# Performance work log

Hardware: AMD Instinct MI355X
Metric: run time of the kernel (lower is better)

## Reference

```python
import jax, jax.numpy as jnp
import numpy as np

D_MODEL, FF_DIM = 1024, 2048
N_SHARED, N_ROUTED, TOP_K = 1, 8, 2
BATCH, SEQ = 2, 2048


def setup_inputs() -> dict:
    key = jax.random.key(0)
    ks = jax.random.split(key, 8)
    init = lambda k, shape: (jax.random.normal(k, shape, jnp.float32) * 0.02)
    x = jax.random.normal(ks[0], (BATCH, SEQ, D_MODEL), jnp.float32)
    Wg = init(ks[1], (D_MODEL, N_ROUTED))                 # gate
    Ws1 = init(ks[2], (D_MODEL, FF_DIM))                  # shared expert (N_SHARED=1)
    Ws3 = init(ks[3], (D_MODEL, FF_DIM))
    Ws2 = init(ks[4], (FF_DIM, D_MODEL))
    We1 = init(ks[5], (N_ROUTED, D_MODEL, FF_DIM))        # routed experts, stacked
    We3 = init(ks[6], (N_ROUTED, D_MODEL, FF_DIM))
    We2 = init(ks[7], (N_ROUTED, FF_DIM, D_MODEL))
    return {"x": x, "Wg": Wg, "Ws1": Ws1, "Ws3": Ws3, "Ws2": Ws2,
            "We1": We1, "We3": We3, "We2": We2}


def reference(x, Wg, Ws1, Ws3, Ws2, We1, We3, We2):
    B, S, d = x.shape
    E = Wg.shape[1]
    xf = x.reshape(-1, d)                                  # [T, d]
    T = xf.shape[0]

    # sigmoid gate + top-k, normalized over selected experts
    gates = jax.nn.sigmoid(xf @ Wg)                        # [T, E]
    vals, idx = jax.lax.top_k(gates, TOP_K)                # [T, K]
    vals = vals / vals.sum(axis=-1, keepdims=True)
    # dense per-expert weights (scatter normalized top-k probs)
    w = jnp.zeros((T, E), x.dtype).at[jnp.arange(T)[:, None], idx].add(vals)  # [T, E]

    # shared expert SwiGLU
    shared = (jax.nn.silu(xf @ Ws1) * (xf @ Ws3)) @ Ws2    # [T, d]

    # routed experts: same math as the torch loop (compute all, mask by w)
    h = jax.nn.silu(jnp.einsum('td,edf->tef', xf, We1)) \
        * jnp.einsum('td,edf->tef', xf, We3)               # [T, E, ff]
    routed = jnp.einsum('tef,efd,te->td', h, We2, w)       # [T, d]

    out = (shared + routed) / (N_SHARED + TOP_K)
    return out.reshape(B, S, d)
```

## Files before the change

### kernel.cpp

```cpp
#include <hip/hip_runtime.h>
#include <stdint.h>

#define TTOK 4096
#define DM   1024
#define FF   2048
#define NE   8

typedef __attribute__((ext_vector_type(8))) short short8;
typedef __attribute__((ext_vector_type(8))) unsigned short ushort8;
typedef __attribute__((ext_vector_type(4))) float f32x4;

#define OFF_XB      0ull
#define OFF_WB13    (OFF_XB      + (size_t)TTOK*DM*2)
#define OFF_WB2     (OFF_WB13    + (size_t)9*4096*1024*2)
#define OFF_H       (OFF_WB2     + (size_t)9*1024*2048*2)
#define OFF_CONTRIB (OFF_H       + (size_t)12288*2048*2)
#define OFF_TOPKW   (OFF_CONTRIB + (size_t)8192*1024*4)
#define OFF_TOPKI   (OFF_TOPKW   + (size_t)TTOK*2*4)
#define OFF_SLOTTOK (OFF_TOPKI   + (size_t)TTOK*2*4)
#define OFF_TOKSLOT (OFF_SLOTTOK + (size_t)TTOK*2*4)
#define OFF_COUNTS  (OFF_TOKSLOT + (size_t)TTOK*2*4)
#define WS_NEEDED   (OFF_COUNTS + 256)

#define VMWAIT0() asm volatile("s_waitcnt vmcnt(0)" ::: "memory")
#define BAR()     __builtin_amdgcn_s_barrier()

__device__ __forceinline__ unsigned short f2bf(float f) {
  unsigned u = __float_as_uint(f);
  return (unsigned short)((u + 0x7FFFu + ((u >> 16) & 1u)) >> 16);
}

__device__ __forceinline__ void async16(const void* g, void* l) {
  __builtin_amdgcn_global_load_lds(
      (const __attribute__((address_space(1))) void*)g,
      (__attribute__((address_space(3))) void*)l, 16, 0, 0);
}

__global__ void k_gatecvt(const float* __restrict__ x, const float* __restrict__ Wg,
                          float* __restrict__ topkw, int* __restrict__ topki,
                          unsigned short* __restrict__ xb) {
  int wave = threadIdx.x >> 6;
  int lane = threadIdx.x & 63;
  int t = blockIdx.x * 4 + wave;
  float acc[NE];
#pragma unroll
  for (int e = 0; e < NE; e++) acc[e] = 0.f;
  const float* xr = x + (size_t)t * DM;
  unsigned short* xbr = xb + (size_t)t * DM;
#pragma unroll
  for (int i = 0; i < 4; i++) {
    int k = i * 256 + lane * 4;
    f32x4 xv = *(const f32x4*)(xr + k);
    unsigned short o0 = f2bf(xv[0]), o1 = f2bf(xv[1]), o2 = f2bf(xv[2]), o3 = f2bf(xv[3]);
    unsigned long long pk = (unsigned long long)o0 | ((unsigned long long)o1 << 16) |
                            ((unsigned long long)o2 << 32) | ((unsigned long long)o3 << 48);
    *(unsigned long long*)(xbr + k) = pk;
#pragma unroll
    for (int j = 0; j < 4; j++) {
      const float* wr = Wg + (size_t)(k + j) * NE;
#pragma unroll
      for (int e = 0; e < NE; e++) acc[e] += xv[j] * wr[e];
    }
  }
#pragma unroll
  for (int e = 0; e < NE; e++) {
#pragma unroll
    for (int off = 32; off >= 1; off >>= 1) acc[e] += __shfl_xor(acc[e], off, 64);
  }
  if (lane == 0) {
    float g[NE];
#pragma unroll
    for (int e = 0; e < NE; e++) g[e] = 1.f / (1.f + __expf(-acc[e]));
    int i1 = -1, i2 = -1;
    float m1 = -1e30f, m2 = -1e30f;
#pragma unroll
    for (int e = 0; e < NE; e++) {
      float v = g[e];
      if (v > m1) { m2 = m1; i2 = i1; m1 = v; i1 = e; }
      else if (v > m2) { m2 = v; i2 = e; }
    }
    float s = m1 + m2;
    topkw[t * 2 + 0] = m1 / s;
    topkw[t * 2 + 1] = m2 / s;
    topki[t * 2 + 0] = i1;
    topki[t * 2 + 1] = i2;
  }
}

__global__ void k_route(const int* __restrict__ topki, int* __restrict__ counts_g,
                        int* __restrict__ offs_g, int* __restrict__ slot_token,
                        int* __restrict__ token_slot) {
  __shared__ int cnt[NE], off[NE], fill[NE];
  int tid = threadIdx.x;
  if (tid < NE) { cnt[tid] = 0; fill[tid] = 0; }
  __syncthreads();
  for (int t = tid; t < TTOK; t += 1024) {
    atomicAdd(&cnt[topki[t * 2 + 0]], 1);
    atomicAdd(&cnt[topki[t * 2 + 1]], 1);
  }
  __syncthreads();
  if (tid == 0) {
    int s = 0;
    for (int e = 0; e < NE; e++) { off[e] = s; s += cnt[e]; }
  }
  __syncthreads();
  if (tid < NE) { counts_g[tid] = cnt[tid]; offs_g[tid] = off[tid]; }
  for (int t = tid; t < TTOK; t += 1024) {
#pragma unroll
    for (int k = 0; k < 2; k++) {
      int e = topki[t * 2 + k];
      int pos = atomicAdd(&fill[e], 1);
      int slot = off[e] + pos;
      slot_token[slot] = t;
      token_slot[t * 2 + k] = slot;
    }
  }
}

__global__ void k_t13(const float* __restrict__ We1, const float* __restrict__ We3,
                      const float* __restrict__ Ws1, const float* __restrict__ Ws3,
                      unsigned short* __restrict__ wb13) {
  __shared__ float tile[64][68];
  int z = blockIdx.z;
  unsigned short* dst = wb13 + (size_t)z * 4096 * 1024;
  int r0 = blockIdx.y * 64;
  int c0 = blockIdx.x * 64;
  int tid = threadIdx.x;
  int r = tid >> 2, q = tid & 3;
  int nn = tid >> 2, g = tid & 3;

  const float* srcs[2] = {(blockIdx.z < 8) ? We1 + (size_t)z * DM * FF : Ws1,
                          (blockIdx.z < 8) ? We3 + (size_t)z * DM * FF : Ws3};
#pragma unroll
  for (int m = 0; m < 2; m++) {
    const float* src = srcs[m] + (size_t)(r0 + r) * FF + c0;
#pragma unroll
    for (int i = 0; i < 4; i++)
      *(f32x4*)&tile[r][i * 16 + q * 4] = *(const f32x4*)(src + i * 16 + q * 4);
    __syncthreads();
    int n = c0 + nn;
    int d = ((n >> 4) << 5) + (n & 15) + m * 16;
    ushort8 o0, o1;
#pragma unroll
    for (int j = 0; j < 8; j++) o0[j] = f2bf(tile[g * 16 + j][nn]);
#pragma unroll
    for (int j = 0; j < 8; j++) o1[j] = f2bf(tile[g * 16 + 8 + j][nn]);
    unsigned short* dp = dst + (size_t)d * 1024 + r0 + g * 16;
    *(ushort8*)dp = o0;
    *(ushort8*)(dp + 8) = o1;
    __syncthreads();
  }
}

__global__ void k_t2(const float* __restrict__ We2, const float* __restrict__ Ws2,
                     unsigned short* __restrict__ wb2) {
  __shared__ float tile[64][68];
  int z = blockIdx.z;
  const float* src0 = (z < 8) ? We2 + (size_t)z * FF * DM : Ws2;
  unsigned short* dst = wb2 + (size_t)z * 1024 * 2048;
  int r0 = blockIdx.y * 64;
  int c0 = blockIdx.x * 64;
  int tid = threadIdx.x;
  int r = tid >> 2, q = tid & 3;
  int nn = tid >> 2, g = tid & 3;

  const float* src = src0 + (size_t)(r0 + r) * DM + c0;
#pragma unroll
  for (int i = 0; i < 4; i++)
    *(f32x4*)&tile[r][i * 16 + q * 4] = *(const f32x4*)(src + i * 16 + q * 4);
  __syncthreads();
  ushort8 o0, o1;
#pragma unroll
  for (int j = 0; j < 8; j++) o0[j] = f2bf(tile[g * 16 + j][nn]);
#pragma unroll
  for (int j = 0; j < 8; j++) o1[j] = f2bf(tile[g * 16 + 8 + j][nn]);
  unsigned short* dp = dst + (size_t)(c0 + nn) * 2048 + r0 + g * 16;
  *(ushort8*)dp = o0;
  *(ushort8*)(dp + 8) = o1;
}

template <bool G13, int K, int NBROW>
__global__ __launch_bounds__(256, 2) void k_gemm(
    const unsigned short* __restrict__ A, const unsigned short* __restrict__ B,
    unsigned short* __restrict__ Hout, float* __restrict__ Cout, float* __restrict__ Dout,
    const int* __restrict__ slot_token, const int* __restrict__ offs,
    const int* __restrict__ counts) {
  __shared__ unsigned short As[2][128 * 64];
  __shared__ unsigned short Bs[2][128 * 64];
  const int NT = K / 64;

  int e = blockIdx.z;
  int seg, cnt;
  if (e == 8) { seg = 8192; cnt = 4096; }
  else        { seg = offs[e]; cnt = counts[e]; }
  int m0 = blockIdx.y * 128;
  if (m0 >= cnt) return;
  int bn = blockIdx.x;

  int tid = threadIdx.x, lane = tid & 63, w = tid >> 6;

  int slb = (((lane & 7) ^ (lane >> 3)) << 4);
  const char* asrc[4];
  const char* bsrc[4];
#pragma unroll
  for (int L = 0; L < 4; L++) {
    int row = L * 32 + w * 8 + (lane >> 3);
    int r = m0 + row; if (r > cnt - 1) r = cnt - 1;
    long tok;
    if (G13) tok = (e == 8) ? (long)r : (long)slot_token[seg + r];
    else     tok = (long)(seg + r);
    asrc[L] = (const char*)A + ((size_t)tok * K) * 2 + slb;
    int br = bn * 128 + row;
    bsrc[L] = (const char*)B + (((size_t)e * NBROW + br) * K) * 2 + slb;
  }

#define STAGE(buf, kt) do {                                            \
    _Pragma("unroll")                                                  \
    for (int L = 0; L < 4; L++) {                                      \
      async16(asrc[L] + (size_t)(kt) * 128, &As[buf][0] + L * 2048 + w * 512); \
      async16(bsrc[L] + (size_t)(kt) * 128, &Bs[buf][0] + L * 2048 + w * 512); \
    }                                                                  \
  } while (0)

  int wr = w >> 1, wc = w & 1;
  int rbA = (wr * 64 + (lane & 15)) * 128;
  int rbB = (wc * 64 + (lane & 15)) * 128;
  int sb0 = ((((lane >> 4) + 0) ^ (lane & 7)) << 4);
  int sb1 = ((((lane >> 4) + 4) ^ (lane & 7)) << 4);

  f32x4 acc[4][4];
#pragma unroll
  for (int i = 0; i < 4; i++)
#pragma unroll
    for (int j = 0; j < 4; j++) acc[i][j] = (f32x4){0.f, 0.f, 0.f, 0.f};

#define COMPUTE(LA, LB) do {                                                         \
    short8 Af[4], Bf[4];                                                             \
    _Pragma("unroll")                                                                \
    for (int mi = 0; mi < 4; mi++) Af[mi] = *(const short8*)((LA) + rbA + mi * 2048 + sb0); \
    _Pragma("unroll")                                                                \
    for (int nf = 0; nf < 4; nf++) Bf[nf] = *(const short8*)((LB) + rbB + nf * 2048 + sb0); \
    _Pragma("unroll")                                                                \
    for (int mi = 0; mi < 4; mi++)                                                   \
      _Pragma("unroll")                                                              \
      for (int nf = 0; nf < 4; nf++)                                                 \
        acc[mi][nf] = __builtin_amdgcn_mfma_f32_16x16x32_bf16(Af[mi], Bf[nf], acc[mi][nf], 0, 0, 0); \
    _Pragma("unroll")                                                                \
    for (int mi = 0; mi < 4; mi++) Af[mi] = *(const short8*)((LA) + rbA + mi * 2048 + sb1); \
    _Pragma("unroll")                                                                \
    for (int nf = 0; nf < 4; nf++) Bf[nf] = *(const short8*)((LB) + rbB + nf * 2048 + sb1); \
    _Pragma("unroll")                                                                \
    for (int mi = 0; mi < 4; mi++)                                                   \
      _Pragma("unroll")                                                              \
      for (int nf = 0; nf < 4; nf++)                                                 \
        acc[mi][nf] = __builtin_amdgcn_mfma_f32_16x16x32_bf16(Af[mi], Bf[nf], acc[mi][nf], 0, 0, 0); \
  } while (0)

  STAGE(0, 0);
  VMWAIT0();
  BAR();

  for (int kt = 0; kt < NT - 1; ++kt) {
    STAGE((kt + 1) & 1, kt + 1);
    const char* LA = (const char*)&As[kt & 1][0];
    const char* LB = (const char*)&Bs[kt & 1][0];
    COMPUTE(LA, LB);
    VMWAIT0();
    BAR();
  }
  {
    const char* LA = (const char*)&As[(NT - 1) & 1][0];
    const char* LB = (const char*)&Bs[(NT - 1) & 1][0];
    COMPUTE(LA, LB);
  }
#undef COMPUTE
#undef STAGE

  if (G13) {
#pragma unroll
    for (int mi = 0; mi < 4; mi++)
#pragma unroll
      for (int j = 0; j < 2; j++)
#pragma unroll
        for (int q = 0; q < 4; q++) {
          int rl = wr * 64 + mi * 16 + (lane >> 4) * 4 + q;
          if (m0 + rl < cnt) {
            float s1 = acc[mi][2 * j][q], s3 = acc[mi][2 * j + 1][q];
            float h = (s1 / (1.f + __expf(-s1))) * s3;
            int nrow = bn * 128 + wc * 64 + 2 * j * 16 + (lane & 15);
            int ffcol = ((nrow >> 5) << 4) + (nrow & 15);
            Hout[(size_t)(seg + m0 + rl) * 2048 + ffcol] = f2bf(h);
          }
        }
  } else {
#pragma unroll
    for (int mi = 0; mi < 4; mi++)
#pragma unroll
      for (int nf = 0; nf < 4; nf++)
#pragma unroll
        for (int q = 0; q < 4; q++) {
          int rl = wr * 64 + mi * 16 + (lane >> 4) * 4 + q;
          if (m0 + rl < cnt) {
            int col = bn * 128 + wc * 64 + nf * 16 + (lane & 15);
            if (e == 8) Dout[(size_t)(m0 + rl) * 1024 + col] = acc[mi][nf][q];
            else        Cout[(size_t)(seg + m0 + rl) * 1024 + col] = acc[mi][nf][q];
          }
        }
  }
}

__global__ void k_combine(float* __restrict__ out, const float* __restrict__ contrib,
                          const int* __restrict__ token_slot, const float* __restrict__ topkw) {
  int t = blockIdx.x;
  int c = threadIdx.x * 4;
  int s0 = token_slot[t * 2 + 0], s1 = token_slot[t * 2 + 1];
  float w0 = topkw[t * 2 + 0], w1 = topkw[t * 2 + 1];
  float* po = out + (size_t)t * DM + c;
  const float* p0 = contrib + (size_t)s0 * DM + c;
  const float* p1 = contrib + (size_t)s1 * DM + c;
  f32x4 vo = *(f32x4*)po;
  f32x4 v0 = *(const f32x4*)p0;
  f32x4 v1 = *(const f32x4*)p1;
#pragma unroll
  for (int i = 0; i < 4; i++)
    vo[i] = (vo[i] + w0 * v0[i] + w1 * v1[i]) * (1.f / 3.f);
  *(f32x4*)po = vo;
}

extern "C" void kernel_launch(void* const* d_in, const int* in_sizes, int n_in,
                              void* d_out, int out_size, void* d_ws, size_t ws_size,
                              hipStream_t stream) {
  const float* x   = (const float*)d_in[0];
  const float* Wg  = (const float*)d_in[1];
  const float* Ws1 = (const float*)d_in[2];
  const float* Ws3 = (const float*)d_in[3];
  const float* Ws2 = (const float*)d_in[4];
  const float* We1 = (const float*)d_in[5];
  const float* We3 = (const float*)d_in[6];
  const float* We2 = (const float*)d_in[7];
  float* out = (float*)d_out;

  if (ws_size < WS_NEEDED) return;

  char* w = (char*)d_ws;
  unsigned short* xb   = (unsigned short*)(w + OFF_XB);
  unsigned short* wb13 = (unsigned short*)(w + OFF_WB13);
  unsigned short* wb2  = (unsigned short*)(w + OFF_WB2);
  unsigned short* H    = (unsigned short*)(w + OFF_H);
  float* contrib       = (float*)(w + OFF_CONTRIB);
  float* topkw         = (float*)(w + OFF_TOPKW);
  int* topki           = (int*)(w + OFF_TOPKI);
  int* slot_token      = (int*)(w + OFF_SLOTTOK);
  int* token_slot      = (int*)(w + OFF_TOKSLOT);
  int* counts          = (int*)(w + OFF_COUNTS);
  int* offs            = counts + 16;

  k_gatecvt<<<TTOK / 4, 256, 0, stream>>>(x, Wg, topkw, topki, xb);
  k_route<<<1, 1024, 0, stream>>>(topki, counts, offs, slot_token, token_slot);
  k_t13<<<dim3(FF / 64, DM / 64, 9), 256, 0, stream>>>(We1, We3, Ws1, Ws3, wb13);
  k_t2<<<dim3(DM / 64, FF / 64, 9), 256, 0, stream>>>(We2, Ws2, wb2);

  k_gemm<true, 1024, 4096><<<dim3(32, 32, 9), 256, 0, stream>>>(
      xb, wb13, H, nullptr, nullptr, slot_token, offs, counts);
  k_gemm<false, 2048, 1024><<<dim3(8, 32, 9), 256, 0, stream>>>(
      H, wb2, nullptr, contrib, out, slot_token, offs, counts);

  k_combine<<<TTOK, 256, 0, stream>>>(out, contrib, token_slot, topkw);
}
```

Measured before the change: 325.7 us.

## Enlarge GEMM tiles to 256x256 with 8 waves and phased load/compute pipeline

```diff
diff --git a/kernel.cpp b/kernel.cpp
--- a/kernel.cpp
+++ b/kernel.cpp
@@ -22,8 +22,10 @@
 #define OFF_COUNTS  (OFF_TOKSLOT + (size_t)TTOK*2*4)
 #define WS_NEEDED   (OFF_COUNTS + 256)
 
-#define VMWAIT0() asm volatile("s_waitcnt vmcnt(0)" ::: "memory")
+#define VMWAIT(N) asm volatile("s_waitcnt vmcnt(" #N ")" ::: "memory")
+#define LGKM0()   asm volatile("s_waitcnt lgkmcnt(0)" ::: "memory")
 #define BAR()     __builtin_amdgcn_s_barrier()
+#define SCHED0()  __builtin_amdgcn_sched_barrier(0)
 
 __device__ __forceinline__ unsigned short f2bf(float f) {
   unsigned u = __float_as_uint(f);
@@ -180,128 +182,145 @@
 }
 
 template <bool G13, int K, int NBROW>
-__global__ __launch_bounds__(256, 2) void k_gemm(
+__global__ __launch_bounds__(512, 2) void k_gemm(
     const unsigned short* __restrict__ A, const unsigned short* __restrict__ B,
     unsigned short* __restrict__ Hout, float* __restrict__ Cout, float* __restrict__ Dout,
     const int* __restrict__ slot_token, const int* __restrict__ offs,
     const int* __restrict__ counts) {
-  __shared__ unsigned short As[2][128 * 64];
-  __shared__ unsigned short Bs[2][128 * 64];
+  __shared__ unsigned short lds[2][2][2][8192];
   const int NT = K / 64;
 
   int e = blockIdx.z;
   int seg, cnt;
   if (e == 8) { seg = 8192; cnt = 4096; }
   else        { seg = offs[e]; cnt = counts[e]; }
-  int m0 = blockIdx.y * 128;
+  int m0 = blockIdx.y * 256;
   if (m0 >= cnt) return;
   int bn = blockIdx.x;
 
   int tid = threadIdx.x, lane = tid & 63, w = tid >> 6;
 
-  int slb = (((lane & 7) ^ (lane >> 3)) << 4);
-  const char* asrc[4];
-  const char* bsrc[4];
-#pragma unroll
-  for (int L = 0; L < 4; L++) {
-    int row = L * 32 + w * 8 + (lane >> 3);
-    int r = m0 + row; if (r > cnt - 1) r = cnt - 1;
-    long tok;
-    if (G13) tok = (e == 8) ? (long)r : (long)slot_token[seg + r];
-    else     tok = (long)(seg + r);
-    asrc[L] = (const char*)A + ((size_t)tok * K) * 2 + slb;
-    int br = bn * 128 + row;
-    bsrc[L] = (const char*)B + (((size_t)e * NBROW + br) * K) * 2 + slb;
-  }
-
-#define STAGE(buf, kt) do {                                            \
-    _Pragma("unroll")                                                  \
-    for (int L = 0; L < 4; L++) {                                      \
-      async16(asrc[L] + (size_t)(kt) * 128, &As[buf][0] + L * 2048 + w * 512); \
-      async16(bsrc[L] + (size_t)(kt) * 128, &Bs[buf][0] + L * 2048 + w * 512); \
-    }                                                                  \
+  int srcslot = (((tid & 7) ^ ((tid >> 3) & 7)) << 4);
+  const char* aptr[2][2];
+  const char* bptr[2][2];
+#pragma unroll
+  for (int half = 0; half < 2; half++)
+#pragma unroll
+    for (int j = 0; j < 2; j++) {
+      int rl = half * 128 + j * 64 + (tid >> 3);
+      int r = m0 + rl; if (r > cnt - 1) r = cnt - 1;
+      long tok;
+      if (G13) tok = (e == 8) ? (long)r : (long)slot_token[seg + r];
+      else     tok = (long)(seg + r);
+      aptr[half][j] = (const char*)A + ((size_t)tok * K) * 2 + srcslot;
+      int br = bn * 256 + rl;
+      bptr[half][j] = (const char*)B + (((size_t)e * NBROW + br) * K) * 2 + srcslot;
+    }
+
+#define STG(b, op, half, kt) do {                                           \
+    const char* _p0 = (op ? bptr : aptr)[half][0] + (size_t)(kt) * 128;     \
+    const char* _p1 = (op ? bptr : aptr)[half][1] + (size_t)(kt) * 128;     \
+    async16(_p0, &lds[b][op][half][(size_t)w * 512]);                       \
+    async16(_p1, &lds[b][op][half][4096 + (size_t)w * 512]);                \
   } while (0)
 
-  int wr = w >> 1, wc = w & 1;
-  int rbA = (wr * 64 + (lane & 15)) * 128;
-  int rbB = (wc * 64 + (lane & 15)) * 128;
-  int sb0 = ((((lane >> 4) + 0) ^ (lane & 7)) << 4);
-  int sb1 = ((((lane >> 4) + 4) ^ (lane & 7)) << 4);
-
-  f32x4 acc[4][4];
-#pragma unroll
-  for (int i = 0; i < 4; i++)
+  int wr = w >> 2, wc = w & 3, wch = wc >> 1;
+  int s0 = (((0 + (lane >> 4)) ^ (lane & 7)) << 4);
+  int s1 = (((4 + (lane >> 4)) ^ (lane & 7)) << 4);
+
+  f32x4 acc[8][4];
+#pragma unroll
+  for (int i = 0; i < 8; i++)
 #pragma unroll
     for (int j = 0; j < 4; j++) acc[i][j] = (f32x4){0.f, 0.f, 0.f, 0.f};
 
-#define COMPUTE(LA, LB) do {                                                         \
-    short8 Af[4], Bf[4];                                                             \
-    _Pragma("unroll")                                                                \
-    for (int mi = 0; mi < 4; mi++) Af[mi] = *(const short8*)((LA) + rbA + mi * 2048 + sb0); \
-    _Pragma("unroll")                                                                \
-    for (int nf = 0; nf < 4; nf++) Bf[nf] = *(const short8*)((LB) + rbB + nf * 2048 + sb0); \
-    _Pragma("unroll")                                                                \
-    for (int mi = 0; mi < 4; mi++)                                                   \
-      _Pragma("unroll")                                                              \
-      for (int nf = 0; nf < 4; nf++)                                                 \
-        acc[mi][nf] = __builtin_amdgcn_mfma_f32_16x16x32_bf16(Af[mi], Bf[nf], acc[mi][nf], 0, 0, 0); \
-    _Pragma("unroll")                                                                \
-    for (int mi = 0; mi < 4; mi++) Af[mi] = *(const short8*)((LA) + rbA + mi * 2048 + sb1); \
-    _Pragma("unroll")                                                                \
-    for (int nf = 0; nf < 4; nf++) Bf[nf] = *(const short8*)((LB) + rbB + nf * 2048 + sb1); \
-    _Pragma("unroll")                                                                \
-    for (int mi = 0; mi < 4; mi++)                                                   \
-      _Pragma("unroll")                                                              \
-      for (int nf = 0; nf < 4; nf++)                                                 \
-        acc[mi][nf] = __builtin_amdgcn_mfma_f32_16x16x32_bf16(Af[mi], Bf[nf], acc[mi][nf], 0, 0, 0); \
+  short8 Af[2][2], Bf[4][2];
+
+#define DO_PHASE(LA, LB, qq, STG_STMT, WAIT_STMT) do {                        \
+    if (qq == 0) {                                                            \
+      _Pragma("unroll") for (int nf = 0; nf < 4; nf++) {                      \
+        int rb = ((wc & 1) * 64 + nf * 16 + (lane & 15)) * 128;               \
+        Bf[nf][0] = *(const short8*)((LB) + rb + s0);                         \
+        Bf[nf][1] = *(const short8*)((LB) + rb + s1);                         \
+      }                                                                       \
+    }                                                                         \
+    _Pragma("unroll") for (int m2 = 0; m2 < 2; m2++) {                        \
+      int ra = (((qq) * 2 + m2) * 16 + (lane & 15)) * 128;                    \
+      Af[m2][0] = *(const short8*)((LA) + ra + s0);                           \
+      Af[m2][1] = *(const short8*)((LA) + ra + s1);                           \
+    }                                                                         \
+    STG_STMT;                                                                 \
+    BAR();                                                                    \
+    LGKM0();                                                                  \
+    SCHED0();                                                                 \
+    __builtin_amdgcn_s_setprio(1);                                            \
+    _Pragma("unroll") for (int m2 = 0; m2 < 2; m2++)                          \
+      _Pragma("unroll") for (int nf = 0; nf < 4; nf++) {                      \
+        acc[(qq) * 2 + m2][nf] = __builtin_amdgcn_mfma_f32_16x16x32_bf16(     \
+            Af[m2][0], Bf[nf][0], acc[(qq) * 2 + m2][nf], 0, 0, 0);           \
+        acc[(qq) * 2 + m2][nf] = __builtin_amdgcn_mfma_f32_16x16x32_bf16(     \
+            Af[m2][1], Bf[nf][1], acc[(qq) * 2 + m2][nf], 0, 0, 0);           \
+      }                                                                       \
+    __builtin_amdgcn_s_setprio(0);                                            \
+    WAIT_STMT;                                                                \
+    BAR();                                                                    \
   } while (0)
 
-  STAGE(0, 0);
-  VMWAIT0();
+  STG(0, 1, 0, 0);
+  STG(0, 1, 1, 0);
+  STG(0, 0, 0, 0);
+  STG(0, 0, 1, 0);
+  STG(1, 1, 0, 1);
+  VMWAIT(2);
   BAR();
 
-  for (int kt = 0; kt < NT - 1; ++kt) {
-    STAGE((kt + 1) & 1, kt + 1);
-    const char* LA = (const char*)&As[kt & 1][0];
-    const char* LB = (const char*)&Bs[kt & 1][0];
-    COMPUTE(LA, LB);
-    VMWAIT0();
-    BAR();
-  }
-  {
-    const char* LA = (const char*)&As[(NT - 1) & 1][0];
-    const char* LB = (const char*)&Bs[(NT - 1) & 1][0];
-    COMPUTE(LA, LB);
-  }
-#undef COMPUTE
-#undef STAGE
+  const char* LA0 = (const char*)&lds[0][0][wr][0];
+  const char* LB0 = (const char*)&lds[0][1][wch][0];
+  const char* LA1 = (const char*)&lds[1][0][wr][0];
+  const char* LB1 = (const char*)&lds[1][1][wch][0];
+
+  for (int it = 0; it < NT / 2; ++it) {
+    int t1 = 2 * it + 1;
+    int n2 = (2 * it + 2 < NT) ? 2 * it + 2 : NT - 1;
+    int n3 = (2 * it + 3 < NT) ? 2 * it + 3 : NT - 1;
+    DO_PHASE(LA0, LB0, 0, STG(1, 1, 1, t1), );
+    DO_PHASE(LA0, LB0, 1, STG(1, 0, 0, t1), );
+    DO_PHASE(LA0, LB0, 2, STG(1, 0, 1, t1), );
+    DO_PHASE(LA0, LB0, 3, STG(0, 1, 0, n2), VMWAIT(2));
+    DO_PHASE(LA1, LB1, 0, STG(0, 1, 1, n2), );
+    DO_PHASE(LA1, LB1, 1, STG(0, 0, 0, n2), );
+    DO_PHASE(LA1, LB1, 2, STG(0, 0, 1, n2), );
+    DO_PHASE(LA1, LB1, 3, STG(1, 1, 0, n3), VMWAIT(2));
+  }
+  VMWAIT(0);
+#undef DO_PHASE
+#undef STG
 
   if (G13) {
 #pragma unroll
-    for (int mi = 0; mi < 4; mi++)
+    for (int mi = 0; mi < 8; mi++)
 #pragma unroll
       for (int j = 0; j < 2; j++)
 #pragma unroll
         for (int q = 0; q < 4; q++) {
-          int rl = wr * 64 + mi * 16 + (lane >> 4) * 4 + q;
+          int rl = wr * 128 + mi * 16 + (lane >> 4) * 4 + q;
           if (m0 + rl < cnt) {
-            float s1 = acc[mi][2 * j][q], s3 = acc[mi][2 * j + 1][q];
-            float h = (s1 / (1.f + __expf(-s1))) * s3;
-            int nrow = bn * 128 + wc * 64 + 2 * j * 16 + (lane & 15);
-            int ffcol = ((nrow >> 5) << 4) + (nrow & 15);
+            float s1v = acc[mi][2 * j][q], s3v = acc[mi][2 * j + 1][q];
+            float h = (s1v / (1.f + __expf(-s1v))) * s3v;
+            int ffcol = (bn * 8 + wc * 2 + j) * 16 + (lane & 15);
             Hout[(size_t)(seg + m0 + rl) * 2048 + ffcol] = f2bf(h);
           }
         }
   } else {
 #pragma unroll
-    for (int mi = 0; mi < 4; mi++)
+    for (int mi = 0; mi < 8; mi++)
 #pragma unroll
       for (int nf = 0; nf < 4; nf++)
 #pragma unroll
         for (int q = 0; q < 4; q++) {
-          int rl = wr * 64 + mi * 16 + (lane >> 4) * 4 + q;
+          int rl = wr * 128 + mi * 16 + (lane >> 4) * 4 + q;
           if (m0 + rl < cnt) {
-            int col = bn * 128 + wc * 64 + nf * 16 + (lane & 15);
+            int col = bn * 256 + wc * 64 + nf * 16 + (lane & 15);
             if (e == 8) Dout[(size_t)(m0 + rl) * 1024 + col] = acc[mi][nf][q];
             else        Cout[(size_t)(seg + m0 + rl) * 1024 + col] = acc[mi][nf][q];
           }
@@ -360,9 +379,9 @@
   k_t13<<<dim3(FF / 64, DM / 64, 9), 256, 0, stream>>>(We1, We3, Ws1, Ws3, wb13);
   k_t2<<<dim3(DM / 64, FF / 64, 9), 256, 0, stream>>>(We2, Ws2, wb2);
 
-  k_gemm<true, 1024, 4096><<<dim3(32, 32, 9), 256, 0, stream>>>(
+  k_gemm<true, 1024, 4096><<<dim3(16, 16, 9), 512, 0, stream>>>(
       xb, wb13, H, nullptr, nullptr, slot_token, offs, counts);
-  k_gemm<false, 2048, 1024><<<dim3(8, 32, 9), 256, 0, stream>>>(
+  k_gemm<false, 2048, 1024><<<dim3(4, 16, 9), 512, 0, stream>>>(
       H, wb2, nullptr, contrib, out, slot_token, offs, counts);
 
   k_combine<<<TTOK, 256, 0, stream>>>(out, contrib, token_slot, topkw);
```

New measurement: 320.1 us, median of 2. Within noise of the previous version (-1.7%).
